# Performance work log

Measured on AMD Instinct MI355X. Metric: run time of the kernel, lower is better.

## Reference

```python
import jax, jax.numpy as jnp
import numpy as np

B, L = 4096, 64
H, E, T, S = 512, 256, 256, 128
CT = T + 3            # context feature dim (term_embedding_dim + 3)
R, V = 4096, 256      # n production rules, n symbols
IN = 2 * E + 2 * T + 6 + H + S  # GRUCell input dim = 1670
NEG = -1e9


def setup_inputs() -> dict:
    key = jax.random.key(0)
    ks = jax.random.split(key, 24)
    sc = 0.02
    inp = {
        "s_tm1": jax.random.normal(ks[0], (B, H), jnp.float32),
        "a_tm1": jax.random.normal(ks[1], (B, E), jnp.float32),
        "p_t": jax.random.normal(ks[2], (B, H + E), jnp.float32),
        "symbol_idx": jax.random.randint(ks[3], (B,), 0, V, jnp.int32),
        "env_emb": jax.random.normal(ks[4], (B, L, CT), jnp.float32),
        "env_len": jax.random.randint(ks[5], (B,), 0, L, jnp.int32),
        "lc_emb": jax.random.normal(ks[6], (B, L, CT), jnp.float32),
        "lc_len": jax.random.randint(ks[7], (B,), 0, L, jnp.int32),
        # parameters
        "symbol_table": jax.random.normal(ks[8], (V, S), jnp.float32) * sc,
        "W1": jax.random.normal(ks[9], (H + CT, H), jnp.float32) * sc,
        "b1": jnp.zeros((H,), jnp.float32),
        "W2": jax.random.normal(ks[10], (H,), jnp.float32) * sc,
        "b2": jnp.zeros((), jnp.float32),
        "W_ih": jax.random.normal(ks[11], (IN, 3 * H), jnp.float32) * sc,
        "W_hh": jax.random.normal(ks[12], (H, 3 * H), jnp.float32) * sc,
        "b_ih": jnp.zeros((3 * H,), jnp.float32),
        "b_hh": jnp.zeros((3 * H,), jnp.float32),
        "Wd": jax.random.normal(ks[13], (H, E), jnp.float32) * sc,
        "bd": jnp.zeros((E,), jnp.float32),
        "rule_table": jax.random.normal(ks[14], (R, E), jnp.float32) * sc,
    }
    return inp


def _context_read(state, emb, length, W1, b1, W2, b2):
    # state: [B,H], emb: [B,L,CT], length: [B] -> context [B,CT]
    x = jnp.concatenate([jnp.broadcast_to(state[:, None, :], emb.shape[:2] + (state.shape[-1],)), emb], axis=-1)
    h = jax.nn.relu(jnp.einsum('blk,kh->blh', x, W1) + b1)      # [B,L,H]
    logit = jnp.einsum('blh,h->bl', h, W2) + b2                  # [B,L]
    mask = jnp.arange(emb.shape[1])[None, :] < length[:, None]
    logit = jnp.where(mask, logit, NEG)
    w = jax.nn.softmax(logit, axis=1)                            # [B,L]
    ctx = jnp.einsum('bl,blc->bc', w, emb)                       # [B,CT]
    # ragged empty-context samples use the zero default_context
    return jnp.where((length > 0)[:, None], ctx, 0.0)


def reference(s_tm1, a_tm1, p_t, symbol_idx, env_emb, env_len, lc_emb, lc_len,
              symbol_table, W1, b1, W2, b2, W_ih, W_hh, b_ih, b_hh, Wd, bd, rule_table):
    n_t = symbol_table[symbol_idx]                               # [B,S]
    ctx_env = _context_read(s_tm1, env_emb, env_len, W1, b1, W2, b2)
    ctx_lc = _context_read(s_tm1, lc_emb, lc_len, W1, b1, W2, b2)
    x = jnp.concatenate([a_tm1, p_t, n_t, ctx_env, ctx_lc], axis=-1)  # [B,IN]
    # torch GRUCell
    gx = x @ W_ih + b_ih                                         # [B,3H]
    gh = s_tm1 @ W_hh + b_hh
    xr, xz, xn = jnp.split(gx, 3, axis=-1)
    hr, hz, hn = jnp.split(gh, 3, axis=-1)
    r = jax.nn.sigmoid(xr + hr)
    z = jax.nn.sigmoid(xz + hz)
    n = jnp.tanh(xn + r * hn)
    h_new = (1.0 - z) * n + z * s_tm1                            # [B,H]
    dec = jnp.tanh(h_new @ Wd + bd)                              # [B,E]
    logits = dec @ rule_table.T                                  # [B,R]
    return logits
```

## Files before the change

### kernel.cpp

```cpp
#include <hip/hip_runtime.h>
#include <hip/hip_bf16.h>
#include <stdint.h>
#include <stddef.h>

#define XP 1696
#define KC 288

#define BIG_G   8192
#define TWO_G   4096
#define ONE_G   2048
#define N_GROUP (BIG_G + TWO_G + ONE_G)
#define N_SLOTI (N_GROUP * 4)

typedef __attribute__((ext_vector_type(8))) short bf16x8;
typedef __attribute__((ext_vector_type(4))) float f32x4;

__device__ __forceinline__ unsigned short f32_bf16(float f) {
    union { float f; unsigned int u; } v; v.f = f;
    unsigned int r = v.u + 0x7FFFu + ((v.u >> 16) & 1u);
    return (unsigned short)(r >> 16);
}
__device__ __forceinline__ float bf16_f32(unsigned short u) {
    union { unsigned int u; float f; } v; v.u = ((unsigned int)u) << 16;
    return v.f;
}

__global__ void tpack_kernel(const float* __restrict__ src, unsigned short* __restrict__ dst,
                             int Ksrc, int Nsrc, int Kp, long total) {
    long idx = (long)blockIdx.x * blockDim.x + threadIdx.x;
    if (idx >= total) return;
    int k = (int)(idx / Nsrc);
    int n = (int)(idx - (long)k * Nsrc);
    float v = (k < Ksrc) ? src[(size_t)k * Nsrc + n] : 0.0f;
    dst[(size_t)n * Kp + k] = f32_bf16(v);
}

__global__ void cvt_kernel(const float* __restrict__ src, unsigned short* __restrict__ dst, int total) {
    int idx = blockIdx.x * blockDim.x + threadIdx.x;
    if (idx < total) dst[idx] = f32_bf16(src[idx]);
}

__global__ void xasm_kernel(const float* __restrict__ a_tm1, const float* __restrict__ p_t,
                            const int* __restrict__ sym, const float* __restrict__ symtab,
                            unsigned short* __restrict__ x_out) {
    int idx = blockIdx.x * blockDim.x + threadIdx.x;
    if (idx >= 4096 * XP) return;
    int b = idx / XP, c = idx - b * XP;
    float v;
    if (c < 256)       v = a_tm1[(size_t)b * 256 + c];
    else if (c < 1024) v = p_t[(size_t)b * 768 + (c - 256)];
    else if (c < 1152) v = symtab[(size_t)sym[b] * 128 + (c - 1024)];
    else if (c < 1670) return;
    else v = 0.0f;
    x_out[idx] = f32_bf16(v);
}

__global__ void sinit_kernel(int* __restrict__ s) {
    int i = blockIdx.x * 256 + threadIdx.x;
    if (i < N_SLOTI) s[i] = -1;
    else if (i < N_SLOTI + 3) s[i] = 0;
}

__global__ void sched_kernel(const int* __restrict__ len_env, const int* __restrict__ len_lc,
                             int* __restrict__ slots) {
    int idx = blockIdx.x * blockDim.x + threadIdx.x;
    if (idx >= 8192) return;
    int b = idx >> 1, wh = idx & 1;
    int len = wh ? len_lc[b] : len_env[b];
    int m = (len + 15) >> 4;
    if (m == 0) m = 1;
    if (m > 4) m = 4;
    int* cursors = slots + N_SLOTI;
    int base;
    if (m >= 3)      { int p = atomicAdd(&cursors[0], 1); base = p * 4; }
    else if (m == 2) { int p = atomicAdd(&cursors[1], 1); base = BIG_G * 4 + (p >> 1) * 4 + (p & 1) * 2; }
    else             { int p = atomicAdd(&cursors[2], 1); base = (BIG_G + TWO_G) * 4 + (p >> 2) * 4 + (p & 3); }
    for (int k = 0; k < m; k++) slots[base + k] = idx * 4 + k;
}

template<int ACT, int OUT_BF16>
__global__ __launch_bounds__(256, 2)
void gemm_bt_kernel(const unsigned short* __restrict__ A,
                    const unsigned short* __restrict__ BT,
                    const float* __restrict__ bias,
                    void* __restrict__ Cout,
                    int M, int N, int K)
{
    __shared__ unsigned short a_lds[128 * 32];
    __shared__ unsigned short b_lds[128 * 32];
    const int tid  = threadIdx.x;
    const int lane = tid & 63;
    const int wave = tid >> 6;
    const int wm = wave >> 1, wn = wave & 1;
    const int row0 = blockIdx.y * 128;
    const int col0 = blockIdx.x * 128;

    f32x4 acc[4][4];
    #pragma unroll
    for (int i = 0; i < 4; i++)
        #pragma unroll
        for (int j = 0; j < 4; j++) acc[i][j] = (f32x4){0.f, 0.f, 0.f, 0.f};

    const int fr = lane & 15;
    const int kk = (lane >> 4) * 8;
    const int srow = (lane >> 2);
    const int scol = (lane & 3) * 8;

    for (int k0 = 0; k0 < K; k0 += 32) {
        __syncthreads();
        #pragma unroll
        for (int j = 0; j < 4; j++) {
            const int c = (wave & 1) * 4 + j;
            const unsigned short* gsrc;
            unsigned short* ldst;
            if (wave < 2) {
                gsrc = A  + (size_t)(row0 + c * 16 + srow) * K + k0 + scol;
                ldst = &a_lds[c * 512];
            } else {
                gsrc = BT + (size_t)(col0 + c * 16 + srow) * K + k0 + scol;
                ldst = &b_lds[c * 512];
            }
            __builtin_amdgcn_global_load_lds(
                (const __attribute__((address_space(1))) void*)gsrc,
                (__attribute__((address_space(3))) void*)ldst, 16, 0, 0);
        }
        __syncthreads();

        bf16x8 af[4], bf[4];
        #pragma unroll
        for (int mt = 0; mt < 4; mt++) af[mt] = *(const bf16x8*)&a_lds[(wm * 64 + mt * 16 + fr) * 32 + kk];
        #pragma unroll
        for (int nt = 0; nt < 4; nt++) bf[nt] = *(const bf16x8*)&b_lds[(wn * 64 + nt * 16 + fr) * 32 + kk];
        #pragma unroll
        for (int mt = 0; mt < 4; mt++)
            #pragma unroll
            for (int nt = 0; nt < 4; nt++)
                acc[mt][nt] = __builtin_amdgcn_mfma_f32_16x16x32_bf16(af[mt], bf[nt], acc[mt][nt], 0, 0, 0);
    }

    const int fq = lane >> 4;
    #pragma unroll
    for (int mt = 0; mt < 4; mt++)
        #pragma unroll
        for (int nt = 0; nt < 4; nt++) {
            int cg = col0 + wn * 64 + nt * 16 + fr;
            float bv = bias ? bias[cg] : 0.0f;
            #pragma unroll
            for (int i = 0; i < 4; i++) {
                int rg = row0 + wm * 64 + mt * 16 + fq * 4 + i;
                float v = acc[mt][nt][i] + bv;
                if (ACT == 1) v = tanhf(v);
                if (OUT_BF16) ((unsigned short*)Cout)[(size_t)rg * N + cg] = f32_bf16(v);
                else          ((float*)Cout)[(size_t)rg * N + cg] = v;
            }
        }
}

__global__ __launch_bounds__(512, 4)
void ctx_kernel(const float* __restrict__ emb_env, const float* __restrict__ emb_lc,
                const int* __restrict__ len_env, const int* __restrict__ len_lc,
                const float* __restrict__ s_proj,
                const unsigned short* __restrict__ W1eT,
                const float* __restrict__ W2, const float* __restrict__ b2,
                const int* __restrict__ slots,
                unsigned short* __restrict__ x_out)
{
    const int g = blockIdx.x;
    const int4 dv = *reinterpret_cast<const int4*>(slots + (size_t)g * 4);
    if (dv.x < 0) return;
    int d[4] = {dv.x, dv.y, dv.z, dv.w};

    __shared__ unsigned short emb_lds[64][296];
    __shared__ float partial_lds[8][64];
    __shared__ float w_lds[64];

    const int tid = threadIdx.x;
    const int lane = tid & 63;
    const int wave = tid >> 6;
    const int fr = lane & 15;
    const int fq = lane >> 4;
    const float b2v = b2[0];

    {
        const int sl = tid >> 7;
        const int t  = tid & 127;
        const int ds = d[sl];
        int nrows = 0;
        const float* src = nullptr;
        if (ds >= 0) {
            int it = ds >> 2, tix = ds & 3;
            int b = it >> 1, wh = it & 1;
            int len = (wh ? len_lc : len_env)[b];
            nrows = len - tix * 16;
            if (nrows > 16) nrows = 16;
            if (nrows < 0) nrows = 0;
            src = (wh ? emb_lc : emb_env) + ((size_t)b * 64 + tix * 16) * 259;
        }
        for (int q = t; q < 16 * 37; q += 128) {
            int r = q / 37, c = 259 + (q - (q / 37) * 37);
            emb_lds[sl * 16 + r][c] = 0;
        }
        const int nf4 = (nrows * 259 + 3) >> 2;
        const float4* s4 = reinterpret_cast<const float4*>(src);
        float4 v[9];
        #pragma unroll
        for (int j = 0; j < 9; j++) {
            int q = t + j * 128;
            if (q < nf4) v[j] = s4[q];
        }
        #pragma unroll
        for (int j = 0; j < 9; j++) {
            int q = t + j * 128;
            if (q < nf4) {
                float fv[4] = {v[j].x, v[j].y, v[j].z, v[j].w};
                int e0 = q * 4;
                #pragma unroll
                for (int jj = 0; jj < 4; jj++) {
                    int e = e0 + jj;
                    int r = e / 259;
                    int c = e - r * 259;
                    emb_lds[sl * 16 + r][c] = f32_bf16(fv[jj]);
                }
            }
        }
    }
    __syncthreads();

    f32x4 acc[4][4];
    #pragma unroll
    for (int i = 0; i < 4; i++)
        #pragma unroll
        for (int j = 0; j < 4; j++) acc[i][j] = (f32x4){0.f, 0.f, 0.f, 0.f};

    #pragma unroll
    for (int ks = 0; ks < 9; ks++) {
        bf16x8 bfr[4];
        #pragma unroll
        for (int nt = 0; nt < 4; nt++) {
            int n = wave * 64 + nt * 16 + fr;
            bfr[nt] = *(const bf16x8*)(W1eT + (size_t)n * KC + ks * 32 + fq * 8);
        }
        bf16x8 af[4];
        #pragma unroll
        for (int mt = 0; mt < 4; mt++)
            af[mt] = *(const bf16x8*)&emb_lds[mt * 16 + fr][ks * 32 + fq * 8];
        __builtin_amdgcn_s_setprio(1);
        #pragma unroll
        for (int nt = 0; nt < 4; nt++)
            #pragma unroll
            for (int mt = 0; mt < 4; mt++)
                acc[mt][nt] = __builtin_amdgcn_mfma_f32_16x16x32_bf16(af[mt], bfr[nt], acc[mt][nt], 0, 0, 0);
        __builtin_amdgcn_s_setprio(0);
    }

    int bslot[4];
    #pragma unroll
    for (int mt = 0; mt < 4; mt++) bslot[mt] = d[mt] >= 0 ? (d[mt] >> 3) : -1;

    float wv[4];
    #pragma unroll
    for (int nt = 0; nt < 4; nt++) wv[nt] = W2[wave * 64 + nt * 16 + fr];

    float plog[4][4];
    #pragma unroll
    for (int mt = 0; mt < 4; mt++)
        #pragma unroll
        for (int ii = 0; ii < 4; ii++) plog[mt][ii] = 0.f;
    #pragma unroll
    for (int nt = 0; nt < 4; nt++) {
        int n = wave * 64 + nt * 16 + fr;
        #pragma unroll
        for (int mt = 0; mt < 4; mt++) {
            if (bslot[mt] < 0) continue;
            float sp = s_proj[(size_t)bslot[mt] * 512 + n];
            #pragma unroll
            for (int ii = 0; ii < 4; ii++) {
                float h = acc[mt][nt][ii] + sp;
                h = fmaxf(h, 0.f);
                plog[mt][ii] += h * wv[nt];
            }
        }
    }
    #pragma unroll
    for (int mt = 0; mt < 4; mt++) {
        if (bslot[mt] < 0) continue;
        #pragma unroll
        for (int ii = 0; ii < 4; ii++) {
            float v = plog[mt][ii];
            v += __shfl_xor(v, 1); v += __shfl_xor(v, 2);
            v += __shfl_xor(v, 4); v += __shfl_xor(v, 8);
            if (fr == 0) partial_lds[wave][mt * 16 + fq * 4 + ii] = v;
        }
    }
    __syncthreads();

    if (wave < 4) {
        int dh = d[wave];
        if (dh >= 0 && (dh & 3) == 0) {
            int it = dh >> 2;
            int b = it >> 1, wh = it & 1;
            int len = (wh ? len_lc : len_env)[b];
            int m = (len + 15) >> 4; if (m == 0) m = 1;
            float logit = -1e9f;
            if (lane < 16 * m && lane < len) {
                logit = b2v;
                #pragma unroll
                for (int w = 0; w < 8; w++) logit += partial_lds[w][wave * 16 + lane];
            }
            float mx = logit;
            #pragma unroll
            for (int off = 1; off < 64; off <<= 1) mx = fmaxf(mx, __shfl_xor(mx, off));
            float e = __expf(logit - mx);
            float s = e;
            #pragma unroll
            for (int off = 1; off < 64; off <<= 1) s += __shfl_xor(s, off);
            if (lane < 16 * m) w_lds[wave * 16 + lane] = e / s;
        }
    }
    __syncthreads();

    #pragma unroll
    for (int g4 = 0; g4 < 4; g4++) {
        int dh = d[g4];
        if (dh < 0 || (dh & 3) != 0) continue;
        int it = dh >> 2;
        int b = it >> 1, wh = it & 1;
        int len = (wh ? len_lc : len_env)[b];
        int xoff = wh ? 1411 : 1152;
        if (tid < 259) {
            const int c = tid;
            const int base = g4 * 16;
            float a0 = 0.f, a1 = 0.f, a2 = 0.f, a3 = 0.f;
            int l = 0;
            for (; l + 3 < len; l += 4) {
                a0 += w_lds[base + l]     * bf16_f32(emb_lds[base + l][c]);
                a1 += w_lds[base + l + 1] * bf16_f32(emb_lds[base + l + 1][c]);
                a2 += w_lds[base + l + 2] * bf16_f32(emb_lds[base + l + 2][c]);
                a3 += w_lds[base + l + 3] * bf16_f32(emb_lds[base + l + 3][c]);
            }
            for (; l < len; l++) a0 += w_lds[base + l] * bf16_f32(emb_lds[base + l][c]);
            x_out[(size_t)b * XP + xoff + c] = f32_bf16((a0 + a1) + (a2 + a3));
        }
    }
}

__global__ void gru_kernel(const float* __restrict__ gx, const float* __restrict__ gh,
                           const float* __restrict__ s, unsigned short* __restrict__ h_b) {
    int idx = blockIdx.x * blockDim.x + threadIdx.x;
    if (idx >= 4096 * 512) return;
    int b = idx >> 9, c = idx & 511;
    const float* gxb = gx + (size_t)b * 1536;
    const float* ghb = gh + (size_t)b * 1536;
    float xr = gxb[c], xz = gxb[c + 512], xn = gxb[c + 1024];
    float hr = ghb[c], hz = ghb[c + 512], hn = ghb[c + 1024];
    float r = 1.f / (1.f + __expf(-(xr + hr)));
    float z = 1.f / (1.f + __expf(-(xz + hz)));
    float n = tanhf(xn + r * hn);
    float h = (1.f - z) * n + z * s[idx];
    h_b[idx] = f32_bf16(h);
}

extern "C" void kernel_launch(void* const* d_in, const int* in_sizes, int n_in,
                              void* d_out, int out_size, void* d_ws, size_t ws_size,
                              hipStream_t stream) {
    const float* s_tm1   = (const float*)d_in[0];
    const float* a_tm1   = (const float*)d_in[1];
    const float* p_t     = (const float*)d_in[2];
    const int*   sym     = (const int*)d_in[3];
    const float* env_emb = (const float*)d_in[4];
    const int*   env_len = (const int*)d_in[5];
    const float* lc_emb  = (const float*)d_in[6];
    const int*   lc_len  = (const int*)d_in[7];
    const float* symtab  = (const float*)d_in[8];
    const float* W1      = (const float*)d_in[9];
    const float* b1      = (const float*)d_in[10];
    const float* W2      = (const float*)d_in[11];
    const float* b2      = (const float*)d_in[12];
    const float* W_ih    = (const float*)d_in[13];
    const float* W_hh    = (const float*)d_in[14];
    const float* b_ih    = (const float*)d_in[15];
    const float* b_hh    = (const float*)d_in[16];
    const float* Wd      = (const float*)d_in[17];
    const float* bd      = (const float*)d_in[18];
    const float* rule    = (const float*)d_in[19];

    char* w = (char*)d_ws;
    float* s_proj = (float*)w;              w += (size_t)4096 * 512 * 4;
    unsigned short* W1sT  = (unsigned short*)w; w += (size_t)512 * 512 * 2;
    unsigned short* W1eT  = (unsigned short*)w; w += (size_t)512 * KC * 2;
    unsigned short* WihT  = (unsigned short*)w; w += (size_t)1536 * XP * 2;
    unsigned short* WhhT  = (unsigned short*)w; w += (size_t)1536 * 512 * 2;
    unsigned short* WdT   = (unsigned short*)w; w += (size_t)256 * 512 * 2;
    unsigned short* ruleb = (unsigned short*)w; w += (size_t)4096 * 256 * 2;
    unsigned short* s_b   = (unsigned short*)w; w += (size_t)4096 * 512 * 2;
    unsigned short* x_b   = (unsigned short*)w; w += (size_t)4096 * XP * 2;
    unsigned short* h_b   = (unsigned short*)w; w += (size_t)4096 * 512 * 2;
    unsigned short* dec_b = (unsigned short*)w; w += (size_t)4096 * 256 * 2;
    int* slots = (int*)w;                   w += (size_t)(N_SLOTI + 8) * 4;

    float* out_f = (float*)d_out;
    float* gx = out_f;
    float* gh = out_f + (size_t)4096 * 1536;

    sinit_kernel<<<(N_SLOTI + 3 + 255) / 256, 256, 0, stream>>>(slots);
    sched_kernel<<<32, 256, 0, stream>>>(env_len, lc_len, slots);

    tpack_kernel<<<(512 * 512 + 255) / 256, 256, 0, stream>>>(W1, W1sT, 512, 512, 512, (long)512 * 512);
    tpack_kernel<<<(512 * KC + 255) / 256, 256, 0, stream>>>(W1 + (size_t)512 * 512, W1eT, 259, 512, KC, (long)512 * KC);
    tpack_kernel<<<(1536 * XP + 255) / 256, 256, 0, stream>>>(W_ih, WihT, 1670, 1536, XP, (long)1536 * XP);
    tpack_kernel<<<(1536 * 512 + 255) / 256, 256, 0, stream>>>(W_hh, WhhT, 512, 1536, 512, (long)1536 * 512);
    tpack_kernel<<<(256 * 512 + 255) / 256, 256, 0, stream>>>(Wd, WdT, 512, 256, 512, (long)256 * 512);
    cvt_kernel<<<4096, 256, 0, stream>>>(rule, ruleb, 4096 * 256);
    cvt_kernel<<<8192, 256, 0, stream>>>(s_tm1, s_b, 4096 * 512);
    xasm_kernel<<<(4096 * XP + 255) / 256, 256, 0, stream>>>(a_tm1, p_t, sym, symtab, x_b);

    gemm_bt_kernel<0, 0><<<dim3(4, 32), 256, 0, stream>>>(s_b, W1sT, b1, s_proj, 4096, 512, 512);

    ctx_kernel<<<N_GROUP, 512, 0, stream>>>(env_emb, lc_emb, env_len, lc_len,
                                            s_proj, W1eT, W2, b2, slots, x_b);

    gemm_bt_kernel<0, 0><<<dim3(12, 32), 256, 0, stream>>>(x_b, WihT, b_ih, gx, 4096, 1536, XP);
    gemm_bt_kernel<0, 0><<<dim3(12, 32), 256, 0, stream>>>(s_b, WhhT, b_hh, gh, 4096, 1536, 512);
    gru_kernel<<<8192, 256, 0, stream>>>(gx, gh, s_tm1, h_b);

    gemm_bt_kernel<1, 1><<<dim3(2, 32), 256, 0, stream>>>(h_b, WdT, bd, dec_b, 4096, 256, 512);

    gemm_bt_kernel<0, 0><<<dim3(32, 32), 256, 0, stream>>>(dec_b, ruleb, nullptr, out_f, 4096, 4096, 256);
}
```

Baseline: 436.4 us.

## Fold W_hh GEMM and weight packing into the context kernel launch

Merges the s_tm1·W_hh GEMM, the W_ih/Wd transpose-packs and the rule-table conversion into the ctx kernel as extra leading blocks of one grid. Independent work can then fill the idle CUs left by the ragged context blocks, and four kernel launches go away. In exchange the GEMM blocks run at 512 threads with two tiles per block inside the ctx kernel's resource limits. The fused W_ih packing uses a strided scattered-write loop rather than a dedicated kernel.

```diff
diff --git a/kernel.cpp b/kernel.cpp
--- a/kernel.cpp
+++ b/kernel.cpp
@@ -11,6 +11,10 @@
 #define ONE_G   2048
 #define N_GROUP (BIG_G + TWO_G + ONE_G)
 #define N_SLOTI (N_GROUP * 4)
+
+#define NGH 192
+#define NAUX 512
+#define CTX_OFF (NGH + NAUX)
 
 typedef __attribute__((ext_vector_type(8))) short bf16x8;
 typedef __attribute__((ext_vector_type(4))) float f32x4;
@@ -157,28 +161,124 @@
 }
 
 __global__ __launch_bounds__(512, 4)
-void ctx_kernel(const float* __restrict__ emb_env, const float* __restrict__ emb_lc,
-                const int* __restrict__ len_env, const int* __restrict__ len_lc,
-                const float* __restrict__ s_proj,
-                const unsigned short* __restrict__ W1eT,
-                const float* __restrict__ W2, const float* __restrict__ b2,
-                const int* __restrict__ slots,
-                unsigned short* __restrict__ x_out)
+void ctx_fused_kernel(const float* __restrict__ emb_env, const float* __restrict__ emb_lc,
+                      const int* __restrict__ len_env, const int* __restrict__ len_lc,
+                      const float* __restrict__ s_proj,
+                      const unsigned short* __restrict__ W1eT,
+                      const float* __restrict__ W2, const float* __restrict__ b2,
+                      const int* __restrict__ slots,
+                      unsigned short* __restrict__ x_out,
+                      const unsigned short* __restrict__ s_b,
+                      const unsigned short* __restrict__ WhhT,
+                      const float* __restrict__ b_hh,
+                      float* __restrict__ gh,
+                      const float* __restrict__ W_ih, unsigned short* __restrict__ WihT,
+                      const float* __restrict__ Wd,   unsigned short* __restrict__ WdT,
+                      const float* __restrict__ rule, unsigned short* __restrict__ ruleb)
 {
-    const int g = blockIdx.x;
-    const int4 dv = *reinterpret_cast<const int4*>(slots + (size_t)g * 4);
-    if (dv.x < 0) return;
-    int d[4] = {dv.x, dv.y, dv.z, dv.w};
-
-    __shared__ unsigned short emb_lds[64][296];
-    __shared__ float partial_lds[8][64];
-    __shared__ float w_lds[64];
-
+    __shared__ __attribute__((aligned(16))) char smem[40192];
     const int tid = threadIdx.x;
     const int lane = tid & 63;
     const int wave = tid >> 6;
     const int fr = lane & 15;
     const int fq = lane >> 4;
+
+    if (blockIdx.x < NGH) {
+        const int half = wave >> 2;
+        const int w4 = wave & 3;
+        const int wm = w4 >> 1, wn = w4 & 1;
+        const int t = blockIdx.x * 2 + half;
+        const int col0 = (t % 12) * 128;
+        const int row0 = (t / 12) * 128;
+        unsigned short* a_lds = (unsigned short*)(smem + half * 16384);
+        unsigned short* b_lds = a_lds + 4096;
+
+        f32x4 acc[4][4];
+        #pragma unroll
+        for (int i = 0; i < 4; i++)
+            #pragma unroll
+            for (int j = 0; j < 4; j++) acc[i][j] = (f32x4){0.f, 0.f, 0.f, 0.f};
+
+        const int kk = (lane >> 4) * 8;
+        const int srow = (lane >> 2);
+        const int scol = (lane & 3) * 8;
+        const int K = 512;
+
+        for (int k0 = 0; k0 < K; k0 += 32) {
+            __syncthreads();
+            #pragma unroll
+            for (int j = 0; j < 4; j++) {
+                const int c = (w4 & 1) * 4 + j;
+                const unsigned short* gsrc;
+                unsigned short* ldst;
+                if (w4 < 2) {
+                    gsrc = s_b  + (size_t)(row0 + c * 16 + srow) * K + k0 + scol;
+                    ldst = &a_lds[c * 512];
+                } else {
+                    gsrc = WhhT + (size_t)(col0 + c * 16 + srow) * K + k0 + scol;
+                    ldst = &b_lds[c * 512];
+                }
+                __builtin_amdgcn_global_load_lds(
+                    (const __attribute__((address_space(1))) void*)gsrc,
+                    (__attribute__((address_space(3))) void*)ldst, 16, 0, 0);
+            }
+            __syncthreads();
+
+            bf16x8 af[4], bf[4];
+            #pragma unroll
+            for (int mt = 0; mt < 4; mt++) af[mt] = *(const bf16x8*)&a_lds[(wm * 64 + mt * 16 + fr) * 32 + kk];
+            #pragma unroll
+            for (int nt = 0; nt < 4; nt++) bf[nt] = *(const bf16x8*)&b_lds[(wn * 64 + nt * 16 + fr) * 32 + kk];
+            #pragma unroll
+            for (int mt = 0; mt < 4; mt++)
+                #pragma unroll
+                for (int nt = 0; nt < 4; nt++)
+                    acc[mt][nt] = __builtin_amdgcn_mfma_f32_16x16x32_bf16(af[mt], bf[nt], acc[mt][nt], 0, 0, 0);
+        }
+
+        #pragma unroll
+        for (int mt = 0; mt < 4; mt++)
+            #pragma unroll
+            for (int nt = 0; nt < 4; nt++) {
+                int cg = col0 + wn * 64 + nt * 16 + fr;
+                float bv = b_hh[cg];
+                #pragma unroll
+                for (int i = 0; i < 4; i++) {
+                    int rg = row0 + wm * 64 + mt * 16 + fq * 4 + i;
+                    gh[(size_t)rg * 1536 + cg] = acc[mt][nt][i] + bv;
+                }
+            }
+        return;
+    }
+
+    if (blockIdx.x < CTX_OFF) {
+        const long stride = (long)NAUX * 512;
+        long base = (long)(blockIdx.x - NGH) * 512 + tid;
+        for (long q = base; q < (long)XP * 1536; q += stride) {
+            int k = (int)(q / 1536);
+            int n = (int)(q - (long)k * 1536);
+            float v = (k < 1670) ? W_ih[(size_t)k * 1536 + n] : 0.0f;
+            WihT[(size_t)n * XP + k] = f32_bf16(v);
+        }
+        for (long q = base; q < (long)512 * 256; q += stride) {
+            int k = (int)(q / 256);
+            int n = (int)(q - (long)k * 256);
+            WdT[(size_t)n * 512 + k] = f32_bf16(Wd[(size_t)k * 256 + n]);
+        }
+        for (long q = base; q < (long)4096 * 256; q += stride)
+            ruleb[q] = f32_bf16(rule[q]);
+        return;
+    }
+
+    const int g = blockIdx.x - CTX_OFF;
+    const int4 dv = *reinterpret_cast<const int4*>(slots + (size_t)g * 4);
+    if (dv.x < 0) return;
+    int d[4] = {dv.x, dv.y, dv.z, dv.w};
+
+    unsigned short (*emb_lds)[296] = (unsigned short(*)[296])smem;
+    float (*partial_lds)[64] = (float(*)[64])(smem + 37888);
+    float* w_lds = (float*)(smem + 37888 + 2048);
+
     const float b2v = b2[0];
 
     {
@@ -407,20 +507,18 @@
 
     tpack_kernel<<<(512 * 512 + 255) / 256, 256, 0, stream>>>(W1, W1sT, 512, 512, 512, (long)512 * 512);
     tpack_kernel<<<(512 * KC + 255) / 256, 256, 0, stream>>>(W1 + (size_t)512 * 512, W1eT, 259, 512, KC, (long)512 * KC);
-    tpack_kernel<<<(1536 * XP + 255) / 256, 256, 0, stream>>>(W_ih, WihT, 1670, 1536, XP, (long)1536 * XP);
     tpack_kernel<<<(1536 * 512 + 255) / 256, 256, 0, stream>>>(W_hh, WhhT, 512, 1536, 512, (long)1536 * 512);
-    tpack_kernel<<<(256 * 512 + 255) / 256, 256, 0, stream>>>(Wd, WdT, 512, 256, 512, (long)256 * 512);
-    cvt_kernel<<<4096, 256, 0, stream>>>(rule, ruleb, 4096 * 256);
     cvt_kernel<<<8192, 256, 0, stream>>>(s_tm1, s_b, 4096 * 512);
     xasm_kernel<<<(4096 * XP + 255) / 256, 256, 0, stream>>>(a_tm1, p_t, sym, symtab, x_b);
 
     gemm_bt_kernel<0, 0><<<dim3(4, 32), 256, 0, stream>>>(s_b, W1sT, b1, s_proj, 4096, 512, 512);
 
-    ctx_kernel<<<N_GROUP, 512, 0, stream>>>(env_emb, lc_emb, env_len, lc_len,
-                                            s_proj, W1eT, W2, b2, slots, x_b);
+    ctx_fused_kernel<<<CTX_OFF + N_GROUP, 512, 0, stream>>>(
+        env_emb, lc_emb, env_len, lc_len, s_proj, W1eT, W2, b2, slots, x_b,
+        s_b, WhhT, b_hh, gh,
+        W_ih, WihT, Wd, WdT, rule, ruleb);
 
     gemm_bt_kernel<0, 0><<<dim3(12, 32), 256, 0, stream>>>(x_b, WihT, b_ih, gx, 4096, 1536, XP);
-    gemm_bt_kernel<0, 0><<<dim3(12, 32), 256, 0, stream>>>(s_b, WhhT, b_hh, gh, 4096, 1536, 512);
     gru_kernel<<<8192, 256, 0, stream>>>(gx, gh, s_tm1, h_b);
 
     gemm_bt_kernel<1, 1><<<dim3(2, 32), 256, 0, stream>>>(h_b, WdT, bd, dec_b, 4096, 256, 512);
```

After: 431.9 us. No clear change (-1.0%).
